# Optimization experiments

Measured on AMD Instinct MI355X. Metric: run time of the kernel, lower is better.

The kernel has to match this reference:

```python
import jax, jax.numpy as jnp
import numpy as np

EPS = 1e-12  # torch F.normalize clamp_min eps

def _l2_normalize(x):
    n = jnp.linalg.norm(x, axis=-1, keepdims=True)
    return x / jnp.maximum(n, EPS)

def setup_inputs() -> dict:
    key = jax.random.key(0)
    k1, k2 = jax.random.split(key)
    z_e = jax.random.normal(k1, (32, 256, 32, 32), dtype=jnp.float32)
    weight = jax.random.normal(k2, (1024, 256), dtype=jnp.float32)
    return {"z_e": z_e, "weight": weight}

def reference(z_e, weight):
    B, C, H, W = z_e.shape  # C == embedding_dim
    z = jnp.transpose(z_e, (0, 2, 3, 1))            # [B,H,W,C]
    flat = _l2_normalize(z.reshape(-1, C))          # [N,C]
    w_n = _l2_normalize(weight)                     # [K,C]
    # distances = 2 - 2 * <flat, w_n>; computed without grad in original
    dist = 2.0 - 2.0 * jnp.matmul(flat, w_n.T)      # [N,K]
    idx = jnp.argmin(dist, axis=1)                  # [N]
    z_q = w_n[idx].reshape(B, H, W, C)              # gather codebook rows
    z_q = jnp.transpose(z_q, (0, 3, 1, 2))          # [B,C,H,W]
    indices = idx.reshape(B, H, W)
    return z_q, indices
```

## Files before the change

### kernel.cpp

```cpp
#include <hip/hip_runtime.h>


typedef _Float16 half8 __attribute__((ext_vector_type(8)));
typedef float floatx4 __attribute__((ext_vector_type(4)));

#define C_DIM 256
#define K_CODES 1024
#define HW 1024
#define NPIX 32768
#define LO_SCALE 2048.0f
#define LO_INV   (1.0f/2048.0f)
#define LDS_STRIDE 40

__global__ __launch_bounds__(256) void vq_norm_w(const float* __restrict__ w,
                                                 float* __restrict__ w_n,
                                                 _Float16* __restrict__ wh,
                                                 _Float16* __restrict__ wl) {
    const int row = blockIdx.x;
    const int t   = threadIdx.x;
    float x = w[row * C_DIM + t];
    float s = x * x;
    #pragma unroll
    for (int off = 32; off > 0; off >>= 1) s += __shfl_down(s, off, 64);
    __shared__ float wsum[4];
    if ((t & 63) == 0) wsum[t >> 6] = s;
    __syncthreads();
    float tot = wsum[0] + wsum[1] + wsum[2] + wsum[3];
    float inv = 1.0f / fmaxf(sqrtf(tot), 1e-12f);
    float y = x * inv;
    w_n[row * C_DIM + t] = y;
    _Float16 hi = (_Float16)y;
    wh[row * C_DIM + t] = hi;
    wl[row * C_DIM + t] = (_Float16)((y - (float)hi) * LO_SCALE);
}

__global__ __launch_bounds__(256) void vq_split_z(const float* __restrict__ z,
                                                  _Float16* __restrict__ zh,
                                                  _Float16* __restrict__ zl) {
    __shared__ float tile[64][65];
    const int t  = threadIdx.x;
    const int pt = blockIdx.x;
    const int ct = blockIdx.y;
    const int b  = blockIdx.z;
    const float* zb = z + ((size_t)b * C_DIM + ct * 64) * HW + pt * 64;
    const int rr = t >> 4, pp = (t & 15) * 4;
    #pragma unroll
    for (int pass = 0; pass < 4; pass++) {
        float4 v = *(const float4*)(zb + (size_t)(pass * 16 + rr) * HW + pp);
        *(float4*)&tile[pass * 16 + rr][pp] = v;
    }
    __syncthreads();
    const int pl = t >> 2;
    const size_t pix = (size_t)b * HW + pt * 64 + pl;
    #pragma unroll
    for (int pass = 0; pass < 2; pass++) {
        const int c0 = ((t & 3) + 4 * pass) * 8;
        half8 hi, lo;
        #pragma unroll
        for (int j = 0; j < 8; j++) {
            float x = tile[c0 + j][pl];
            _Float16 h = (_Float16)x;
            hi[j] = h;
            lo[j] = (_Float16)((x - (float)h) * LO_SCALE);
        }
        *(half8*)(zh + pix * C_DIM + ct * 64 + c0) = hi;
        *(half8*)(zl + pix * C_DIM + ct * 64 + c0) = lo;
    }
}

__global__ __launch_bounds__(256, 2) void vq_gemm(
        const _Float16* __restrict__ zh, const _Float16* __restrict__ zl,
        const _Float16* __restrict__ wh, const _Float16* __restrict__ wl,
        float* __restrict__ cand_val, int* __restrict__ cand_idx) {
    __shared__ _Float16 Ah[128 * LDS_STRIDE];
    __shared__ _Float16 Al[128 * LDS_STRIDE];
    __shared__ _Float16 Bh[128 * LDS_STRIDE];
    __shared__ _Float16 Bl[128 * LDS_STRIDE];
    __shared__ float red_v[128][2];
    __shared__ int   red_i[128][2];

    const int tid  = threadIdx.x;
    const int lane = tid & 63, wave = tid >> 6;
    const int wm = wave >> 1, wn = wave & 1;
    const int quad = lane >> 4, l15 = lane & 15;
    const int m0 = blockIdx.x * 128, n0 = blockIdx.y * 128;

    const int sr  = tid >> 2;
    const int sc  = (tid & 3) * 8;
    const int sr1 = sr + 64;

    floatx4 acc_h[4][4], acc_x[4][4];
    #pragma unroll
    for (int i = 0; i < 4; i++)
        #pragma unroll
        for (int j = 0; j < 4; j++) {
            acc_h[i][j] = (floatx4){0.f, 0.f, 0.f, 0.f};
            acc_x[i][j] = (floatx4){0.f, 0.f, 0.f, 0.f};
        }

    const int aoff = (wm * 64 + l15) * LDS_STRIDE + quad * 8;
    const int boff = (wn * 64 + l15) * LDS_STRIDE + quad * 8;
    const int l0 = sr  * LDS_STRIDE + sc;
    const int l1 = sr1 * LDS_STRIDE + sc;

    for (int kt = 0; kt < 8; kt++) {
        const int k0 = kt * 32;
        const size_t ga0 = (size_t)(m0 + sr ) * C_DIM + k0 + sc;
        const size_t ga1 = (size_t)(m0 + sr1) * C_DIM + k0 + sc;
        const size_t gb0 = (size_t)(n0 + sr ) * C_DIM + k0 + sc;
        const size_t gb1 = (size_t)(n0 + sr1) * C_DIM + k0 + sc;
        uint4 vah0 = *(const uint4*)(zh + ga0);
        uint4 vah1 = *(const uint4*)(zh + ga1);
        uint4 val0 = *(const uint4*)(zl + ga0);
        uint4 val1 = *(const uint4*)(zl + ga1);
        uint4 vbh0 = *(const uint4*)(wh + gb0);
        uint4 vbh1 = *(const uint4*)(wh + gb1);
        uint4 vbl0 = *(const uint4*)(wl + gb0);
        uint4 vbl1 = *(const uint4*)(wl + gb1);
        __syncthreads();
        *(uint4*)&Ah[l0] = vah0;  *(uint4*)&Ah[l1] = vah1;
        *(uint4*)&Al[l0] = val0;  *(uint4*)&Al[l1] = val1;
        *(uint4*)&Bh[l0] = vbh0;  *(uint4*)&Bh[l1] = vbh1;
        *(uint4*)&Bl[l0] = vbl0;  *(uint4*)&Bl[l1] = vbl1;
        __syncthreads();

        half8 ah[4], al[4], bh[4], bl[4];
        #pragma unroll
        for (int i = 0; i < 4; i++) {
            ah[i] = *(const half8*)&Ah[aoff + i * 16 * LDS_STRIDE];
            al[i] = *(const half8*)&Al[aoff + i * 16 * LDS_STRIDE];
            bh[i] = *(const half8*)&Bh[boff + i * 16 * LDS_STRIDE];
            bl[i] = *(const half8*)&Bl[boff + i * 16 * LDS_STRIDE];
        }
        #pragma unroll
        for (int mi = 0; mi < 4; mi++)
            #pragma unroll
            for (int ni = 0; ni < 4; ni++) {
                acc_h[mi][ni] = __builtin_amdgcn_mfma_f32_16x16x32_f16(ah[mi], bh[ni], acc_h[mi][ni], 0, 0, 0);
                acc_x[mi][ni] = __builtin_amdgcn_mfma_f32_16x16x32_f16(ah[mi], bl[ni], acc_x[mi][ni], 0, 0, 0);
                acc_x[mi][ni] = __builtin_amdgcn_mfma_f32_16x16x32_f16(al[mi], bh[ni], acc_x[mi][ni], 0, 0, 0);
            }
    }

    #pragma unroll
    for (int mi = 0; mi < 4; mi++) {
        #pragma unroll
        for (int r = 0; r < 4; r++) {
            float bv = -__builtin_inff();
            int   bi = 0x7fffffff;
            #pragma unroll
            for (int ni = 0; ni < 4; ni++) {
                float v = acc_h[mi][ni][r] + acc_x[mi][ni][r] * LO_INV;
                int  ci = n0 + wn * 64 + ni * 16 + l15;
                if (v > bv || (v == bv && ci < bi)) { bv = v; bi = ci; }
            }
            #pragma unroll
            for (int mk = 8; mk; mk >>= 1) {
                float ov = __shfl_xor(bv, mk, 16);
                int   oi = __shfl_xor(bi, mk, 16);
                if (ov > bv || (ov == bv && oi < bi)) { bv = ov; bi = oi; }
            }
            if (l15 == 0) {
                int row = wm * 64 + mi * 16 + quad * 4 + r;
                red_v[row][wn] = bv;
                red_i[row][wn] = bi;
            }
        }
    }
    __syncthreads();
    if (tid < 128) {
        float bv = red_v[tid][0]; int bi = red_i[tid][0];
        float v2 = red_v[tid][1]; int i2 = red_i[tid][1];
        if (v2 > bv || (v2 == bv && i2 < bi)) { bv = v2; bi = i2; }
        const int pix = m0 + tid;
        cand_val[(size_t)pix * 8 + blockIdx.y] = bv;
        cand_idx[(size_t)pix * 8 + blockIdx.y] = bi;
    }
}

__global__ __launch_bounds__(256) void vq_finalize(
        const float* __restrict__ cand_val,
        const int*   __restrict__ cand_idx,
        const float* __restrict__ w_n,
        float* __restrict__ zq,
        float* __restrict__ idx_out) {
    const int n = blockIdx.x * 256 + threadIdx.x;
    const size_t base = (size_t)n * 8;
    float bv = cand_val[base];
    int   bi = cand_idx[base];
    #pragma unroll
    for (int t = 1; t < 8; t++) {
        float v = cand_val[base + t];
        int   c = cand_idx[base + t];
        if (v > bv || (v == bv && c < bi)) { bv = v; bi = c; }
    }
    idx_out[n] = (float)bi;
    const int b = n >> 10;
    const int p = n & 1023;
    float* zqb = zq + (size_t)b * (C_DIM * HW) + p;
    const float* wr = w_n + (size_t)bi * C_DIM;
    #pragma unroll 4
    for (int c = 0; c < C_DIM; c += 4) {
        float4 wv = *(const float4*)(wr + c);
        zqb[(size_t)(c + 0) * HW] = wv.x;
        zqb[(size_t)(c + 1) * HW] = wv.y;
        zqb[(size_t)(c + 2) * HW] = wv.z;
        zqb[(size_t)(c + 3) * HW] = wv.w;
    }
}

extern "C" void kernel_launch(void* const* d_in, const int* in_sizes, int n_in,
                              void* d_out, int out_size, void* d_ws, size_t ws_size,
                              hipStream_t stream) {
    const float* z = (const float*)d_in[0];
    const float* w = (const float*)d_in[1];
    float* out     = (float*)d_out;

    char* ws = (char*)d_ws;
    float*    w_n  = (float*)(ws);
    _Float16* wh   = (_Float16*)(ws + (1u << 20));
    _Float16* wl   = (_Float16*)(ws + (3u << 19));
    _Float16* zh   = (_Float16*)(ws + (2u << 20));
    _Float16* zl   = (_Float16*)(ws + 18874368u);
    float*    cval = (float*)(ws + 35651584u);
    int*      cidx = (int*)(ws + 36700160u);

    vq_norm_w<<<K_CODES, 256, 0, stream>>>(w, w_n, wh, wl);
    vq_split_z<<<dim3(16, 4, 32), 256, 0, stream>>>(z, zh, zl);
    vq_gemm<<<dim3(NPIX / 128, K_CODES / 128), 256, 0, stream>>>(zh, zl, wh, wl, cval, cidx);
    vq_finalize<<<NPIX / 256, 256, 0, stream>>>(cval, cidx, w_n, out, out + 8388608);
}
```

Measured before the change: 191.7 us.

## Load GEMM tiles directly into LDS with global_load_lds in fragment-major layout

Replaces the register-staged global-to-LDS copy in the split-fp16 GEMM with direct global_load_lds DMA. Each wave now loads one of the four operand arrays (zh, zl, wh, wl) into its own LDS buffer in an MFMA-fragment-ordered layout. The K tile grows from 32 to 64, which halves the number of barrier pairs, and fragment reads become contiguous per lane with no padding. This is meant to cut VGPR pressure and the instructions spent on staging stores and bank-conflict padding. In exchange LDS use rises to 64KB per block, which may limit the two-blocks-per-CU occupancy, and there is still no double buffering.

Measured after the change: 202.6 us. 5.6% more time.

```diff
diff --git a/kernel.cpp b/kernel.cpp
--- a/kernel.cpp
+++ b/kernel.cpp
@@ -10,7 +10,10 @@
 #define NPIX 32768
 #define LO_SCALE 2048.0f
 #define LO_INV   (1.0f/2048.0f)
-#define LDS_STRIDE 40
+
+#define GLOAD_LDS16(g, l) __builtin_amdgcn_global_load_lds(                    \
+    (const __attribute__((address_space(1))) unsigned int*)(g),                \
+    (__attribute__((address_space(3))) unsigned int*)(l), 16, 0, 0)
 
 __global__ __launch_bounds__(256) void vq_norm_w(const float* __restrict__ w,
                                                  float* __restrict__ w_n,
@@ -72,10 +75,7 @@
         const _Float16* __restrict__ zh, const _Float16* __restrict__ zl,
         const _Float16* __restrict__ wh, const _Float16* __restrict__ wl,
         float* __restrict__ cand_val, int* __restrict__ cand_idx) {
-    __shared__ _Float16 Ah[128 * LDS_STRIDE];
-    __shared__ _Float16 Al[128 * LDS_STRIDE];
-    __shared__ _Float16 Bh[128 * LDS_STRIDE];
-    __shared__ _Float16 Bl[128 * LDS_STRIDE];
+    __shared__ _Float16 lds[4][8192];
     __shared__ float red_v[128][2];
     __shared__ int   red_i[128][2];
 
@@ -85,9 +85,11 @@
     const int quad = lane >> 4, l15 = lane & 15;
     const int m0 = blockIdx.x * 128, n0 = blockIdx.y * 128;
 
-    const int sr  = tid >> 2;
-    const int sc  = (tid & 3) * 8;
-    const int sr1 = sr + 64;
+    const _Float16* psrc = (wave == 0) ? zh : (wave == 1) ? zl
+                         : (wave == 2) ? wh : wl;
+    const int row0 = (wave < 2) ? m0 : n0;
+    const _Float16* gbase = psrc + (size_t)(row0 + l15) * C_DIM + quad * 8;
+    _Float16* ldsw = &lds[wave][0];
 
     floatx4 acc_h[4][4], acc_x[4][4];
     #pragma unroll
@@ -98,48 +100,36 @@
             acc_x[i][j] = (floatx4){0.f, 0.f, 0.f, 0.f};
         }
 
-    const int aoff = (wm * 64 + l15) * LDS_STRIDE + quad * 8;
-    const int boff = (wn * 64 + l15) * LDS_STRIDE + quad * 8;
-    const int l0 = sr  * LDS_STRIDE + sc;
-    const int l1 = sr1 * LDS_STRIDE + sc;
-
-    for (int kt = 0; kt < 8; kt++) {
-        const int k0 = kt * 32;
-        const size_t ga0 = (size_t)(m0 + sr ) * C_DIM + k0 + sc;
-        const size_t ga1 = (size_t)(m0 + sr1) * C_DIM + k0 + sc;
-        const size_t gb0 = (size_t)(n0 + sr ) * C_DIM + k0 + sc;
-        const size_t gb1 = (size_t)(n0 + sr1) * C_DIM + k0 + sc;
-        uint4 vah0 = *(const uint4*)(zh + ga0);
-        uint4 vah1 = *(const uint4*)(zh + ga1);
-        uint4 val0 = *(const uint4*)(zl + ga0);
-        uint4 val1 = *(const uint4*)(zl + ga1);
-        uint4 vbh0 = *(const uint4*)(wh + gb0);
-        uint4 vbh1 = *(const uint4*)(wh + gb1);
-        uint4 vbl0 = *(const uint4*)(wl + gb0);
-        uint4 vbl1 = *(const uint4*)(wl + gb1);
+    const int afrag = wm * 4, bfrag = wn * 4;
+
+    for (int kt = 0; kt < 4; kt++) {
         __syncthreads();
-        *(uint4*)&Ah[l0] = vah0;  *(uint4*)&Ah[l1] = vah1;
-        *(uint4*)&Al[l0] = val0;  *(uint4*)&Al[l1] = val1;
-        *(uint4*)&Bh[l0] = vbh0;  *(uint4*)&Bh[l1] = vbh1;
-        *(uint4*)&Bl[l0] = vbl0;  *(uint4*)&Bl[l1] = vbl1;
+        const _Float16* g = gbase + kt * 64;
+        #pragma unroll
+        for (int u = 0; u < 16; u++) {
+            GLOAD_LDS16(g + (u >> 1) * (16 * C_DIM) + (u & 1) * 32,
+                        ldsw + u * 512);
+        }
         __syncthreads();
-
-        half8 ah[4], al[4], bh[4], bl[4];
-        #pragma unroll
-        for (int i = 0; i < 4; i++) {
-            ah[i] = *(const half8*)&Ah[aoff + i * 16 * LDS_STRIDE];
-            al[i] = *(const half8*)&Al[aoff + i * 16 * LDS_STRIDE];
-            bh[i] = *(const half8*)&Bh[boff + i * 16 * LDS_STRIDE];
-            bl[i] = *(const half8*)&Bl[boff + i * 16 * LDS_STRIDE];
-        }
-        #pragma unroll
-        for (int mi = 0; mi < 4; mi++)
-            #pragma unroll
-            for (int ni = 0; ni < 4; ni++) {
-                acc_h[mi][ni] = __builtin_amdgcn_mfma_f32_16x16x32_f16(ah[mi], bh[ni], acc_h[mi][ni], 0, 0, 0);
-                acc_x[mi][ni] = __builtin_amdgcn_mfma_f32_16x16x32_f16(ah[mi], bl[ni], acc_x[mi][ni], 0, 0, 0);
-                acc_x[mi][ni] = __builtin_amdgcn_mfma_f32_16x16x32_f16(al[mi], bh[ni], acc_x[mi][ni], 0, 0, 0);
-            }
+        #pragma unroll
+        for (int s = 0; s < 2; s++) {
+            half8 ah[4], al[4], bh[4], bl[4];
+            #pragma unroll
+            for (int i = 0; i < 4; i++) {
+                ah[i] = *(const half8*)&lds[0][((afrag + i) * 2 + s) * 512 + lane * 8];
+                al[i] = *(const half8*)&lds[1][((afrag + i) * 2 + s) * 512 + lane * 8];
+                bh[i] = *(const half8*)&lds[2][((bfrag + i) * 2 + s) * 512 + lane * 8];
+                bl[i] = *(const half8*)&lds[3][((bfrag + i) * 2 + s) * 512 + lane * 8];
+            }
+            #pragma unroll
+            for (int mi = 0; mi < 4; mi++)
+                #pragma unroll
+                for (int ni = 0; ni < 4; ni++) {
+                    acc_h[mi][ni] = __builtin_amdgcn_mfma_f32_16x16x32_f16(ah[mi], bh[ni], acc_h[mi][ni], 0, 0, 0);
+                    acc_x[mi][ni] = __builtin_amdgcn_mfma_f32_16x16x32_f16(ah[mi], bl[ni], acc_x[mi][ni], 0, 0, 0);
+                    acc_x[mi][ni] = __builtin_amdgcn_mfma_f32_16x16x32_f16(al[mi], bh[ni], acc_x[mi][ni], 0, 0, 0);
+                }
+        }
     }
 
     #pragma unroll
```
